# Performance work log

Hardware: AMD Instinct MI355X
Metric: run time of the kernel (lower is better)

## Reference

```python
import jax, jax.numpy as jnp
import numpy as np

B, N, D, P = 8, 16384, 64, 100


def setup_inputs() -> dict:
    key = jax.random.key(0)
    k1, k2, k3 = jax.random.split(key, 3)
    x = jax.random.normal(k1, (B, N, D), dtype=jnp.float32)
    y = jax.random.normal(k2, (B, N, D), dtype=jnp.float32)
    # the torch loop draws randn(d) per projection; stack them as [P, d]
    theta = jax.random.normal(k3, (P, D), dtype=jnp.float32)
    eps = jnp.ones((1,), dtype=jnp.float32)  # unused on sliced path
    return {"x": x, "y": y, "theta": theta, "eps": eps, "n_projections": P}


def reference(x, y, theta, eps, n_projections):
    # Sliced-OT path of SlicedOptimalTransport.transport (memory check selects it).
    # Normalize each projection direction (F.normalize(theta, dim=0) per draw).
    theta_n = theta / jnp.linalg.norm(theta, axis=-1, keepdims=True)  # [P, d]
    n_proj = theta_n.shape[0]

    # Project all points onto all directions at once (vectorizes the torch loop).
    x_proj = jnp.einsum("bnd,pd->bpn", x, theta_n)  # [B, P, N]
    y_proj = jnp.einsum("bnd,pd->bpn", y, theta_n)  # [B, P, N]

    # torch: _, x_indices = sort(x_proj); y_sorted = sort(y_proj);
    #        transported_proj.scatter_(1, x_indices, y_sorted)
    # i.e. transported_proj[j] = y_sorted[rank of x_proj[j]].
    y_sorted = jnp.sort(y_proj, axis=-1)
    rank = jnp.argsort(jnp.argsort(x_proj, axis=-1), axis=-1)  # rank of each point
    transported_proj = jnp.take_along_axis(y_sorted, rank, axis=-1)  # [B, P, N]

    diff = transported_proj - x_proj  # [B, P, N]
    # accumulate diff_proj * theta over all projections, then average
    transported = jnp.einsum("bpn,pd->bnd", diff, theta_n)  # [B, N, d]
    return x + transported / n_proj
```

## Files before the change

### kernel.cpp

```cpp
#include <hip/hip_runtime.h>
#include <cstdint>

#define NB    8
#define NN    16384
#define ND    64
#define NP    100
#define NPP   128
#define ST    1024
#define SE    16
#define TROW  72

typedef __attribute__((ext_vector_type(8))) short short8;
typedef __attribute__((ext_vector_type(4))) float f32x4;

__device__ __forceinline__ short bf16c(float f) {
  uint32_t u = __float_as_uint(f);
  u = u + 0x7FFFu + ((u >> 16) & 1u);
  return (short)(u >> 16);
}
__device__ __forceinline__ uint32_t bf16pk(float a, float b) {
  return (uint32_t)(ushort)bf16c(a) | ((uint32_t)(ushort)bf16c(b) << 16);
}

__device__ __forceinline__ uint32_t f2s_u(uint32_t s) {
  return s ^ (((uint32_t)((int32_t)s >> 31)) | 0x80000000u);
}
__device__ __forceinline__ float s2f(uint32_t u) {
  uint32_t m = (u & 0x80000000u) ? 0x80000000u : 0xFFFFFFFFu;
  return __uint_as_float(u ^ m);
}

__device__ __forceinline__ uint32_t swz(uint32_t w) {
  return w ^ ((w >> 3) & 0x1Cu);
}

__device__ __forceinline__ void radix_pass(uint32_t (&k)[SE], uint32_t* S,
                                           uint32_t* WG, int tid, int sh,
                                           bool first) {
  const int lane = tid & 63;
  const int wave = tid >> 6;

  if (!first) {
#pragma unroll
    for (int q = 0; q < 4; q++) {
      uint32_t wb = ((uint32_t)tid << 4) + ((uint32_t)q << 2);
      uint4 v = *(const uint4*)(S + (wb ^ ((wb >> 3) & 0x1Cu)));
      k[4 * q + 0] = v.x; k[4 * q + 1] = v.y;
      k[4 * q + 2] = v.z; k[4 * q + 3] = v.w;
    }
  }

  uint64_t c = 0;
#pragma unroll
  for (int e = 0; e < SE; e++) {
    uint32_t d = (k[e] >> sh) & 7u;
    c += 1ull << (d << 3);
  }

  uint32_t lo = (uint32_t)c, hi = (uint32_t)(c >> 32);
  uint32_t h[4], o[4];
  h[0] = (lo & 0xFFu) | ((lo & 0xFF00u) << 8);
  h[1] = ((lo >> 16) & 0xFFu) | ((lo >> 24) << 16);
  h[2] = (hi & 0xFFu) | ((hi & 0xFF00u) << 8);
  h[3] = ((hi >> 16) & 0xFFu) | ((hi >> 24) << 16);
#pragma unroll
  for (int i = 0; i < 4; i++) o[i] = h[i];

#pragma unroll
  for (int off = 1; off <= 32; off <<= 1) {
#pragma unroll
    for (int i = 0; i < 4; i++) {
      uint32_t t = __shfl_up(h[i], (unsigned)off, 64);
      if (lane >= off) h[i] += t;
    }
  }

  if (lane == 63) {
#pragma unroll
    for (int i = 0; i < 4; i++) WG[(wave << 2) + i] = h[i];
  }
  __syncthreads();

  if (tid < 64) {
    uint32_t v = WG[tid];
    uint32_t own = v;
#pragma unroll
    for (int off = 4; off <= 32; off <<= 1) {
      uint32_t t = __shfl_up(v, (unsigned)off, 64);
      if (tid >= off) v += t;
    }
    uint32_t wexcl = v - own;
    uint32_t grand = __shfl(v, 60 + (tid & 3), 64);
    uint32_t gl = grand & 0xFFFFu, gh = grand >> 16;
    uint32_t ps = gl + gh, pincl = ps;
#pragma unroll
    for (int off = 1; off <= 2; off <<= 1) {
      uint32_t t = __shfl_up(pincl, (unsigned)off, 64);
      if ((tid & 3) >= off) pincl += t;
    }
    uint32_t pexcl = pincl - ps;
    uint32_t g0 = pexcl + (wexcl & 0xFFFFu);
    uint32_t g1 = pexcl + gl + (wexcl >> 16);
    WG[tid] = g0 | (g1 << 16);
  }
  __syncthreads();

  uint32_t p0 = WG[(wave << 2) + 0] + (h[0] - o[0]);
  uint32_t p1 = WG[(wave << 2) + 1] + (h[1] - o[1]);
  uint32_t p2 = WG[(wave << 2) + 2] + (h[2] - o[2]);
  uint32_t p3 = WG[(wave << 2) + 3] + (h[3] - o[3]);
  uint64_t pc0 = (uint64_t)p0 | ((uint64_t)p1 << 32);
  uint64_t pc1 = (uint64_t)p2 | ((uint64_t)p3 << 32);

#pragma unroll
  for (int e = 0; e < SE; e++) {
    uint32_t d = (k[e] >> sh) & 7u;
    uint32_t s16 = (d & 3u) << 4;
    bool lo4 = d < 4u;
    uint64_t t = lo4 ? pc0 : pc1;
    uint32_t pos = (uint32_t)(t >> s16) & 0xFFFFu;
    uint64_t inc = 1ull << s16;
    pc0 += lo4 ? inc : 0ull;
    pc1 += lo4 ? 0ull : inc;
    S[swz(pos)] = k[e];
  }
  __syncthreads();
}

__device__ __forceinline__ void radix18(uint32_t (&k)[SE], uint32_t* S,
                                        uint32_t* WG, int tid) {
  bool first = true;
  for (int sh = 14; sh < 32; sh += 3) {
    radix_pass(k, S, WG, tid, sh, first);
    first = false;
  }
}

__global__ void normalize_theta(const float* __restrict__ theta,
                                ushort* __restrict__ thb,
                                ushort* __restrict__ thbT) {
  const int p = blockIdx.x, t = threadIdx.x;
  ushort v16 = 0;
  if (p < NP) {
    float v = theta[p * ND + t];
    float ss = v * v;
#pragma unroll
    for (int off = 32; off >= 1; off >>= 1) ss += __shfl_xor(ss, off, 64);
    v16 = (ushort)bf16c(v * rsqrtf(ss));
  }
  thb[p * ND + t] = v16;
  thbT[t * NPP + p] = v16;
}

__global__ __launch_bounds__(256) void project_mfma(
    const float* __restrict__ x, const float* __restrict__ y,
    const ushort* __restrict__ thb, float* __restrict__ xp,
    float* __restrict__ yp) {
  __shared__ ushort XT[64 * TROW];
  __shared__ ushort YT[64 * TROW];
  const int tid  = threadIdx.x;
  const int lane = tid & 63;
  const int quad = lane >> 4;
  const int mloc = lane & 15;
  const int wave = tid >> 6;

  const int m0 = blockIdx.x * 64 + wave * 16;
  const int b  = m0 >> 14;
  const int n0 = m0 & (NN - 1);

  {
    const float4* gx = (const float4*)(x + (long)blockIdx.x * 64 * ND);
    const float4* gy = (const float4*)(y + (long)blockIdx.x * 64 * ND);
#pragma unroll
    for (int i = 0; i < 4; i++) {
      const int f4 = tid + 256 * i;
      const int row = f4 >> 4;
      const int c4  = f4 & 15;
      float4 vx = gx[f4];
      float4 vy = gy[f4];
      uint2 px, py;
      px.x = bf16pk(vx.x, vx.y); px.y = bf16pk(vx.z, vx.w);
      py.x = bf16pk(vy.x, vy.y); py.y = bf16pk(vy.z, vy.w);
      const int us = row * TROW + c4 * 4;
      *(uint2*)(XT + us) = px;
      *(uint2*)(YT + us) = py;
    }
  }
  __syncthreads();

  const int fr = wave * 16 + mloc;
  const short8 ax0 = *(const short8*)(XT + fr * TROW + quad * 8);
  const short8 ax1 = *(const short8*)(XT + fr * TROW + 32 + quad * 8);
  const short8 ay0 = *(const short8*)(YT + fr * TROW + quad * 8);
  const short8 ay1 = *(const short8*)(YT + fr * TROW + 32 + quad * 8);

  const f32x4 zero = {0.f, 0.f, 0.f, 0.f};
#pragma unroll
  for (int t = 0; t < 7; t++) {
    const int p = t * 16 + mloc;
    const short8 b0 = *(const short8*)(thb + p * ND + quad * 8);
    const short8 b1 = *(const short8*)(thb + p * ND + 32 + quad * 8);
    f32x4 accx = __builtin_amdgcn_mfma_f32_16x16x32_bf16(ax0, b0, zero, 0, 0, 0);
    accx = __builtin_amdgcn_mfma_f32_16x16x32_bf16(ax1, b1, accx, 0, 0, 0);
    f32x4 accy = __builtin_amdgcn_mfma_f32_16x16x32_bf16(ay0, b0, zero, 0, 0, 0);
    accy = __builtin_amdgcn_mfma_f32_16x16x32_bf16(ay1, b1, accy, 0, 0, 0);
    if (t < 6 || mloc < (NP - 96)) {
      const long off = ((long)b * NP + p) * NN + n0 + quad * 4;
      *(f32x4*)(xp + off) = accx;
      *(f32x4*)(yp + off) = accy;
    }
  }
}

__global__ __launch_bounds__(ST, 8) void sort_diff_kernel(
    const float* __restrict__ xp, float* __restrict__ yp) {
  __shared__ uint32_t S[NN];
  __shared__ uint32_t WG[64];
  const int tid = threadIdx.x;
  const long sbase = (long)blockIdx.x * NN;
  uint32_t k[SE];

  {
    const uint4* yg = (const uint4*)(yp + sbase) + (tid << 2);
#pragma unroll
    for (int q = 0; q < 4; q++) {
      uint4 v = yg[q];
      k[4 * q + 0] = f2s_u(v.x); k[4 * q + 1] = f2s_u(v.y);
      k[4 * q + 2] = f2s_u(v.z); k[4 * q + 3] = f2s_u(v.w);
    }
  }
  radix18(k, S, WG, tid);

  float ys[SE];
#pragma unroll
  for (int q = 0; q < 4; q++) {
    uint32_t wb = ((uint32_t)tid << 4) + ((uint32_t)q << 2);
    uint4 v = *(const uint4*)(S + (wb ^ ((wb >> 3) & 0x1Cu)));
    ys[4 * q + 0] = s2f(v.x); ys[4 * q + 1] = s2f(v.y);
    ys[4 * q + 2] = s2f(v.z); ys[4 * q + 3] = s2f(v.w);
  }

  {
    const uint4* xg = (const uint4*)(xp + sbase) + (tid << 2);
#pragma unroll
    for (int q = 0; q < 4; q++) {
      uint4 v = xg[q];
      uint32_t g = ((uint32_t)tid << 4) + (uint32_t)(q << 2);
      k[4 * q + 0] = (f2s_u(v.x) & 0xFFFFC000u) | (g + 0);
      k[4 * q + 1] = (f2s_u(v.y) & 0xFFFFC000u) | (g + 1);
      k[4 * q + 2] = (f2s_u(v.z) & 0xFFFFC000u) | (g + 2);
      k[4 * q + 3] = (f2s_u(v.w) & 0xFFFFC000u) | (g + 3);
    }
  }
  radix18(k, S, WG, tid);

#pragma unroll
  for (int q = 0; q < 4; q++) {
    uint32_t wb = ((uint32_t)tid << 4) + ((uint32_t)q << 2);
    uint4 v = *(const uint4*)(S + (wb ^ ((wb >> 3) & 0x1Cu)));
    k[4 * q + 0] = v.x & 0x3FFFu; k[4 * q + 1] = v.y & 0x3FFFu;
    k[4 * q + 2] = v.z & 0x3FFFu; k[4 * q + 3] = v.w & 0x3FFFu;
  }
  __syncthreads();

#pragma unroll
  for (int e = 0; e < SE; e++) {
    S[swz(k[e])] = __float_as_uint(ys[e]);
  }
  __syncthreads();

  const uint4* xg = (const uint4*)(xp + sbase) + (tid << 2);
  float4* og = (float4*)(yp + sbase) + (tid << 2);
#pragma unroll
  for (int q = 0; q < 4; q++) {
    uint32_t wb = ((uint32_t)tid << 4) + ((uint32_t)q << 2);
    uint4 v = *(const uint4*)(S + (wb ^ ((wb >> 3) & 0x1Cu)));
    uint4 xb = xg[q];
    float4 o;
    o.x = __uint_as_float(v.x) - __uint_as_float(xb.x);
    o.y = __uint_as_float(v.y) - __uint_as_float(xb.y);
    o.z = __uint_as_float(v.z) - __uint_as_float(xb.z);
    o.w = __uint_as_float(v.w) - __uint_as_float(xb.w);
    og[q] = o;
  }
}

__global__ __launch_bounds__(256) void combine_mfma(
    const float* __restrict__ x, const float* __restrict__ diff,
    const ushort* __restrict__ thbT, float* __restrict__ out) {
  const int tid  = threadIdx.x;
  const int lane = tid & 63;
  const int quad = lane >> 4;
  const int mloc = lane & 15;
  const int wave = tid >> 6;

  const int m0 = blockIdx.x * 64 + wave * 16;
  const int b  = m0 >> 14;
  const int n0 = m0 & (NN - 1);

  const float* dbase = diff + ((long)b * NP) * NN + n0 + mloc;
  short8 a[4];
#pragma unroll
  for (int kf = 0; kf < 4; kf++) {
#pragma unroll
    for (int j = 0; j < 8; j++) {
      const int p = kf * 32 + quad * 8 + j;
      const float v = (p < NP) ? dbase[(long)p * NN] : 0.0f;
      a[kf][j] = bf16c(v);
    }
  }

  const float inv = 1.0f / (float)NP;
  const f32x4 zero = {0.f, 0.f, 0.f, 0.f};
#pragma unroll
  for (int t = 0; t < 4; t++) {
    const int d = t * 16 + mloc;
    f32x4 acc = zero;
#pragma unroll
    for (int kf = 0; kf < 4; kf++) {
      const short8 bf = *(const short8*)(thbT + (long)d * NPP + kf * 32 + quad * 8);
      acc = __builtin_amdgcn_mfma_f32_16x16x32_bf16(a[kf], bf, acc, 0, 0, 0);
    }
#pragma unroll
    for (int r = 0; r < 4; r++) {
      const long off = (long)(m0 + quad * 4 + r) * ND + d;
      out[off] = x[off] + acc[r] * inv;
    }
  }
}

extern "C" void kernel_launch(void* const* d_in, const int* in_sizes, int n_in,
                              void* d_out, int out_size, void* d_ws, size_t ws_size,
                              hipStream_t stream) {
  const float* x     = (const float*)d_in[0];
  const float* y     = (const float*)d_in[1];
  const float* theta = (const float*)d_in[2];
  float* out = (float*)d_out;

  ushort* thb  = (ushort*)d_ws;
  ushort* thbT = thb + (size_t)NPP * ND;
  float* xp = (float*)((char*)d_ws + (1 << 15));
  float* yp = xp + (size_t)NB * NP * NN;

  normalize_theta<<<dim3(NPP), dim3(ND), 0, stream>>>(theta, thb, thbT);
  project_mfma<<<dim3((NB * NN) / 64), dim3(256), 0, stream>>>(x, y, thb, xp, yp);
  sort_diff_kernel<<<dim3(NB * NP), dim3(ST), 0, stream>>>(xp, yp);
  combine_mfma<<<dim3((NB * NN) / 64), dim3(256), 0, stream>>>(x, yp, thbT, out);
}
```

Before: 348.0 us.

## Emit bf16 diff in point-major layout so combine reads contiguous rows

The sort kernel now converts each diff value to bf16 and writes it into a [B, N, 128] point-major buffer that aliases the output buffer. The combine kernel can then load its MFMA A-fragments as contiguous short8 vectors instead of strided fp32 gathers with per-element conversion. This halves the intermediate traffic and removes the strided reads. In exchange the sort kernel makes scattered 2-byte stores with a 256-byte stride. Correctness relies on each wave reading its dT rows before overwriting the same bytes with output.

```diff
diff --git a/kernel.cpp b/kernel.cpp
--- a/kernel.cpp
+++ b/kernel.cpp
@@ -213,11 +213,14 @@
 }
 
 __global__ __launch_bounds__(ST, 8) void sort_diff_kernel(
-    const float* __restrict__ xp, float* __restrict__ yp) {
+    const float* __restrict__ xp, const float* __restrict__ yp,
+    ushort* __restrict__ dT) {
   __shared__ uint32_t S[NN];
   __shared__ uint32_t WG[64];
   const int tid = threadIdx.x;
   const long sbase = (long)blockIdx.x * NN;
+  const int bb = blockIdx.x / NP;
+  const int pp = blockIdx.x - bb * NP;
   uint32_t k[SE];
 
   {
@@ -269,24 +272,23 @@
   }
   __syncthreads();
 
+  ushort* drow = dT + (long)bb * NN * NPP + pp;
   const uint4* xg = (const uint4*)(xp + sbase) + (tid << 2);
-  float4* og = (float4*)(yp + sbase) + (tid << 2);
 #pragma unroll
   for (int q = 0; q < 4; q++) {
     uint32_t wb = ((uint32_t)tid << 4) + ((uint32_t)q << 2);
     uint4 v = *(const uint4*)(S + (wb ^ ((wb >> 3) & 0x1Cu)));
     uint4 xb = xg[q];
-    float4 o;
-    o.x = __uint_as_float(v.x) - __uint_as_float(xb.x);
-    o.y = __uint_as_float(v.y) - __uint_as_float(xb.y);
-    o.z = __uint_as_float(v.z) - __uint_as_float(xb.z);
-    o.w = __uint_as_float(v.w) - __uint_as_float(xb.w);
-    og[q] = o;
+    const long r0 = (long)wb * NPP;
+    drow[r0 + 0 * NPP] = (ushort)bf16c(__uint_as_float(v.x) - __uint_as_float(xb.x));
+    drow[r0 + 1 * NPP] = (ushort)bf16c(__uint_as_float(v.y) - __uint_as_float(xb.y));
+    drow[r0 + 2 * NPP] = (ushort)bf16c(__uint_as_float(v.z) - __uint_as_float(xb.z));
+    drow[r0 + 3 * NPP] = (ushort)bf16c(__uint_as_float(v.w) - __uint_as_float(xb.w));
   }
 }
 
 __global__ __launch_bounds__(256) void combine_mfma(
-    const float* __restrict__ x, const float* __restrict__ diff,
+    const float* __restrict__ x, const ushort* __restrict__ dT,
     const ushort* __restrict__ thbT, float* __restrict__ out) {
   const int tid  = threadIdx.x;
   const int lane = tid & 63;
@@ -295,18 +297,18 @@
   const int wave = tid >> 6;
 
   const int m0 = blockIdx.x * 64 + wave * 16;
-  const int b  = m0 >> 14;
-  const int n0 = m0 & (NN - 1);
-
-  const float* dbase = diff + ((long)b * NP) * NN + n0 + mloc;
+
+  const ushort* abase = dT + (long)(m0 + mloc) * NPP;
   short8 a[4];
 #pragma unroll
   for (int kf = 0; kf < 4; kf++) {
+    a[kf] = *(const short8*)(abase + kf * 32 + quad * 8);
+  }
+  {
+    const int pb = 96 + quad * 8;
 #pragma unroll
     for (int j = 0; j < 8; j++) {
-      const int p = kf * 32 + quad * 8 + j;
-      const float v = (p < NP) ? dbase[(long)p * NN] : 0.0f;
-      a[kf][j] = bf16c(v);
+      if (pb + j >= NP) a[3][j] = 0;
     }
   }
 
@@ -341,9 +343,10 @@
   ushort* thbT = thb + (size_t)NPP * ND;
   float* xp = (float*)((char*)d_ws + (1 << 15));
   float* yp = xp + (size_t)NB * NP * NN;
+  ushort* dT = (ushort*)d_out;
 
   normalize_theta<<<dim3(NPP), dim3(ND), 0, stream>>>(theta, thb, thbT);
   project_mfma<<<dim3((NB * NN) / 64), dim3(256), 0, stream>>>(x, y, thb, xp, yp);
-  sort_diff_kernel<<<dim3(NB * NP), dim3(ST), 0, stream>>>(xp, yp);
-  combine_mfma<<<dim3((NB * NN) / 64), dim3(256), 0, stream>>>(x, yp, thbT, out);
-}
+  sort_diff_kernel<<<dim3(NB * NP), dim3(ST), 0, stream>>>(xp, yp, dT);
+  combine_mfma<<<dim3((NB * NN) / 64), dim3(256), 0, stream>>>(x, dT, thbT, out);
+}
```

After: 458.9 us. +31.9%, slower.
